# Kernel tuning notes

Hardware: AMD Instinct MI355X
Metric: run time of the kernel (lower is better)

Reference implementation:

```python
import jax, jax.numpy as jnp
import numpy as np

N, E, DIN, DOUT, NNZ = 8192, 4096, 256, 128, 65536
TEMP = float(DOUT) ** 0.5
NEG = -1e9


def setup_inputs() -> dict:
    key = jax.random.key(0)
    ks = jax.random.split(key, 8)
    stdv = 1.0 / np.sqrt(DOUT)
    u = lambda k, shp: jax.random.uniform(k, shp, jnp.float32, -stdv, stdv)
    x = jax.random.normal(ks[0], (N, DIN), jnp.float32)
    nodes = jax.random.randint(ks[1], (NNZ,), 0, N, jnp.int32)
    edges = jax.random.randint(ks[2], (NNZ,), 0, E, jnp.int32)
    hyperedge_index = jnp.stack([nodes, edges])  # [2, nnz]
    return {
        "x": x,
        "weight": u(ks[3], (DIN, DOUT)),   # transfer weight
        "weight2": u(ks[4], (DIN, DOUT)),
        "weight3": u(ks[5], (DOUT, DOUT)),
        "bias": u(ks[6], (DOUT,)),
        "q_ctx": u(ks[7], (DOUT,)),        # word_context.weight[0]
        "hyperedge_index": hyperedge_index,
        "num_nodes": N,
        "num_edges": E,
    }


def reference(x, weight, weight2, weight3, bias, q_ctx, hyperedge_index, num_nodes, num_edges):
    # dense incidence H[node, edge] = 1  (hyperedge_preprocess)
    H = jnp.zeros((num_nodes, num_edges), x.dtype).at[
        hyperedge_index[0], hyperedge_index[1]].set(1.0)
    adj = H.T                       # [E, N]  (mask / original attention for attn1)

    x4 = x @ weight2                # [N, D]  x_4att
    xt = x @ weight + bias          # [N, D]  transferred features (v of attn1)

    # ---- attention1: query = shared word-context vector, keys = x4 ----
    row = (q_ctx / TEMP) @ x4.T                    # [N] (q1 rows are identical)
    scores1 = jnp.where(adj == 0, NEG, row[None, :])  # [E, N]
    att1 = jax.nn.softmax(adj, axis=-1) + jax.nn.softmax(scores1, axis=-1)
    edge = att1 @ xt                               # [E, D]

    att2he = att1.T                                # [N, E]

    # ---- attention2: queries = x4, keys = edge @ W3 ----
    edge4 = edge @ weight3                         # [E, D]
    scores2 = jnp.where(adj.T == 0, NEG, (x4 / TEMP) @ edge4.T)  # [N, E]
    att2hn = jax.nn.softmax(adj.T, axis=-1) + jax.nn.softmax(scores2, axis=-1)

    # ---- fused outer-product attention and output projection ----
    A = att2he @ att2he.T + att2hn @ att2hn.T      # [N, N]
    h_prime_g = jax.nn.elu(A @ x4)                 # [N, D]
    return h_prime_g
```

## Files before the change

kernel.cpp:

```cpp
#include <hip/hip_runtime.h>
#include <math.h>

constexpr int Nn   = 8192;
constexpr int Ee   = 4096;
constexpr int DIN  = 256;
constexpr int DOUT = 128;
constexpr int NNZ  = 65536;
constexpr int EC   = 96;
constexpr int NC   = 48;

#define TEMPR 0.08838834764831845f
#define EM1   1.7182818284590452f


typedef __attribute__((ext_vector_type(8))) short short8;
typedef __attribute__((ext_vector_type(4))) float f32x4;

static __device__ __forceinline__ float wave_sum64(float v) {
#pragma unroll
    for (int m = 32; m; m >>= 1) v += __shfl_xor(v, m, 64);
    return v;
}
static __device__ __forceinline__ float wave_max64(float v) {
#pragma unroll
    for (int m = 32; m; m >>= 1) v = fmaxf(v, __shfl_xor(v, m, 64));
    return v;
}
static __device__ __forceinline__ short f2bf(float f) {
    union { float f; unsigned u; } v; v.f = f;
    const unsigned r = (v.u + 0x7FFFu + ((v.u >> 16) & 1u)) >> 16;
    return (short)r;
}
static __device__ __forceinline__ unsigned packbf2(float a, float b) {
    return ((unsigned)(unsigned short)f2bf(a)) |
           (((unsigned)(unsigned short)f2bf(b)) << 16);
}
static __device__ __forceinline__ float2 unpackbf2(unsigned u) {
    union { unsigned u; float f; } lo, hi;
    lo.u = u << 16; hi.u = u & 0xFFFF0000u;
    return make_float2(lo.f, hi.f);
}

__global__ __launch_bounds__(256) void k_ww3(
    const float* __restrict__ W, const float* __restrict__ W2,
    const float* __restrict__ W3, const float* __restrict__ bias,
    short* __restrict__ W2T, short* __restrict__ WWT, float* __restrict__ bW3,
    uint4* __restrict__ zb, unsigned zTot16)
{
    const int b = blockIdx.x;
    const int t = threadIdx.x;
    if (b < 32) {
        __shared__ float sW[8][128];
        const int r0 = b * 8;
        for (int i = t; i < 1024; i += 256)
            sW[i >> 7][i & 127] = W[(size_t)(r0 + (i >> 7)) * DOUT + (i & 127)];
        __syncthreads();
        const int c  = t & 127;
        const int rh = (t >> 7) * 4;
        float acc[4] = {0.f, 0.f, 0.f, 0.f};
        for (int k = 0; k < 128; ++k) {
            const float w3 = W3[(size_t)k * DOUT + c];
#pragma unroll
            for (int i = 0; i < 4; ++i) acc[i] = fmaf(sW[rh + i][k], w3, acc[i]);
        }
#pragma unroll
        for (int i = 0; i < 4; ++i)
            WWT[(size_t)c * DIN + (r0 + rh + i)] = f2bf(acc[i]);
    } else if (b < 40) {
        const int k0 = (b - 32) * 32;
        for (int i = t; i < 32 * 128; i += 256) {
            const int k = k0 + (i >> 7);
            const int n = i & 127;
            W2T[(size_t)n * DIN + k] = f2bf(W2[(size_t)k * DOUT + n]);
        }
    } else if (b == 40) {
        if (t < 128) {
            float acc = 0.f;
            for (int k = 0; k < 128; ++k)
                acc = fmaf(bias[k], W3[(size_t)k * DOUT + t], acc);
            bW3[t] = acc;
        }
    } else {
        uint4 z; z.x = z.y = z.z = z.w = 0u;
        for (unsigned i = (unsigned)(b - 41) * 256u + t; i < zTot16;
             i += 64u * 256u)
            zb[i] = z;
    }
}

__global__ __launch_bounds__(256) void k_gemm1f(
    const float* __restrict__ x, const short* __restrict__ W2T,
    const short* __restrict__ WWT, const float* __restrict__ bW3,
    const float* __restrict__ q, const int* __restrict__ hidx,
    unsigned* __restrict__ bitmap, int* __restrict__ degE, int* __restrict__ degN,
    int* __restrict__ csrEn, int* __restrict__ csrNe, int* __restrict__ csrNs,
    unsigned* __restrict__ x4b, uint2* __restrict__ xfb,
    float* __restrict__ rowv)
{
    __shared__ float srow[16];
    const int t    = threadIdx.x;
    const int lane = t & 63;
    const int wv   = t >> 6;
    const int n16  = lane & 15;
    const int quad = lane >> 4;
    const int r0   = blockIdx.x * 16;
    const int n0   = wv * 32;

    const unsigned gid = blockIdx.x * 256 + t;
    if (gid < NNZ) {
        const int n = hidx[gid];
        const int e = hidx[NNZ + gid];
        const unsigned word = (unsigned)n * (unsigned)Ee + (unsigned)e;
        const unsigned bit  = 1u << (word & 31u);
        const unsigned old  = atomicOr(&bitmap[word >> 5], bit);
        if (!(old & bit)) {
            const int pe = atomicAdd(&degE[e], 1);
            if (pe < EC) {
                csrEn[e * EC + pe] = n;
                const int pn = atomicAdd(&degN[n], 1);
                if (pn < NC) {
                    csrNe[n * NC + pn] = e;
                    csrNs[n * NC + pn] = e * EC + pe;
                }
            }
        }
    }

    f32x4 acc4[2], accw[2];
#pragma unroll
    for (int nt = 0; nt < 2; ++nt) {
        acc4[nt] = (f32x4){0.f, 0.f, 0.f, 0.f};
        accw[nt] = (f32x4){0.f, 0.f, 0.f, 0.f};
    }
#pragma unroll
    for (int k0 = 0; k0 < DIN; k0 += 32) {
        const int kb = k0 + quad * 8;
        const float4 xa = *(const float4*)&x[(size_t)(r0 + n16) * DIN + kb];
        const float4 xb = *(const float4*)&x[(size_t)(r0 + n16) * DIN + kb + 4];
        short8 af;
        af[0] = f2bf(xa.x); af[1] = f2bf(xa.y); af[2] = f2bf(xa.z); af[3] = f2bf(xa.w);
        af[4] = f2bf(xb.x); af[5] = f2bf(xb.y); af[6] = f2bf(xb.z); af[7] = f2bf(xb.w);
#pragma unroll
        for (int nt = 0; nt < 2; ++nt) {
            const int col = n0 + nt * 16 + n16;
            const short8 b4 = *(const short8*)&W2T[(size_t)col * DIN + kb];
            const short8 bw = *(const short8*)&WWT[(size_t)col * DIN + kb];
            acc4[nt] = __builtin_amdgcn_mfma_f32_16x16x32_bf16(af, b4, acc4[nt], 0, 0, 0);
            accw[nt] = __builtin_amdgcn_mfma_f32_16x16x32_bf16(af, bw, accw[nt], 0, 0, 0);
        }
    }

    float bwv[2], qv[2];
#pragma unroll
    for (int nt = 0; nt < 2; ++nt) {
        const int col = n0 + nt * 16 + n16;
        bwv[nt] = bW3[col];
        qv[nt]  = q[col];
    }
    const int s = wv * 16 + n16;
#pragma unroll
    for (int reg = 0; reg < 4; ++reg) {
        const int row = r0 + quad * 4 + reg;
        const unsigned p4 = packbf2(acc4[0][reg], acc4[1][reg]);
        const unsigned pw = packbf2(accw[0][reg] + bwv[0],
                                    accw[1][reg] + bwv[1]);
        x4b[(size_t)row * 64 + s] = p4;
        xfb[(size_t)row * 64 + s] = make_uint2(p4, pw);
    }
    float pr[4];
#pragma unroll
    for (int reg = 0; reg < 4; ++reg)
        pr[reg] = qv[0] * acc4[0][reg] + qv[1] * acc4[1][reg];
#pragma unroll
    for (int m = 8; m; m >>= 1) {
#pragma unroll
        for (int reg = 0; reg < 4; ++reg) pr[reg] += __shfl_xor(pr[reg], m, 64);
    }
    if (t < 16) srow[t] = 0.f;
    __syncthreads();
    if (n16 == 0) {
#pragma unroll
        for (int reg = 0; reg < 4; ++reg) atomicAdd(&srow[quad * 4 + reg], pr[reg]);
    }
    __syncthreads();
    if (t < 16) rowv[r0 + t] = srow[t] * TEMPR;
}

__global__ __launch_bounds__(256) void k_reduxA(
    const uint2* __restrict__ xfb, const int* __restrict__ degE,
    float* __restrict__ csx4, float* __restrict__ csxw, float* __restrict__ c2g)
{
    const int t    = threadIdx.x;
    const int lane = t & 63;
    const int w    = t >> 6;
    const int b    = blockIdx.x;
    float2 a4 = {0.f, 0.f}, aw = {0.f, 0.f};
    for (int k = 0; k < 32; ++k) {
        const int n = b * 128 + w + k * 4;
        const uint2 u = xfb[(size_t)n * 64 + lane];
        const float2 fv = unpackbf2(u.x);
        const float2 tv = unpackbf2(u.y);
        a4.x += fv.x; a4.y += fv.y;
        aw.x += tv.x; aw.y += tv.y;
    }
    atomicAdd(&csx4[lane * 2 + 0], a4.x); atomicAdd(&csx4[lane * 2 + 1], a4.y);
    atomicAdd(&csxw[lane * 2 + 0], aw.x); atomicAdd(&csxw[lane * 2 + 1], aw.y);

    const int gid = b * 256 + t;
    if (gid < Ee) {
        const int de = min(degE[gid], EC);
        const float ue = de ? 1.0f / ((float)Nn + (float)de * EM1)
                            : 2.0f / (float)Nn;
        const float v = wave_sum64(ue * ue);
        if (lane == 0) atomicAdd(c2g, v);
    }
}

__global__ __launch_bounds__(128, 6) void k_edge1(
    const int* __restrict__ degE, const int* __restrict__ csrEn,
    const float* __restrict__ rowv,
    const float* __restrict__ csx4, const float* __restrict__ csxw,
    const uint2* __restrict__ xfb,
    float* __restrict__ Sval, unsigned* __restrict__ e4b, uint2* __restrict__ GGb,
    float* __restrict__ wsArr)
{
    __shared__ int   sN[2][EC];
    __shared__ float sS[2][EC];
    const int t    = threadIdx.x;
    const int w    = t >> 6;
    const int lane = t & 63;
    const int e    = blockIdx.x * 2 + w;
    const int deg  = min(degE[e], EC);
    const float ue = deg ? 1.0f / ((float)Nn + (float)deg * EM1) : 2.0f / (float)Nn;

    int   n0 = 0, n1 = 0;
    float r0 = -INFINITY, r1 = -INFINITY;
    if (lane < deg)      { n0 = csrEn[e * EC + lane];      r0 = rowv[n0]; }
    if (lane + 64 < deg) { n1 = csrEn[e * EC + lane + 64]; r1 = rowv[n1]; }
    const float m  = wave_max64(fmaxf(r0, r1));
    const float e0 = (lane < deg)      ? expf(r0 - m) : 0.f;
    const float e1 = (lane + 64 < deg) ? expf(r1 - m) : 0.f;
    const float Z  = wave_sum64(e0 + e1);
    const float inv = deg ? 1.0f / Z : 0.f;
    const float base = EM1 * ue;
    if (lane < deg) {
        const float sv = fmaf(e0, inv, base);
        sN[w][lane] = n0; sS[w][lane] = sv;
        Sval[e * EC + lane] = sv;
        atomicAdd(&wsArr[n0], ue * sv);
    }
    if (lane + 64 < deg) {
        const float sv = fmaf(e1, inv, base);
        sN[w][lane + 64] = n1; sS[w][lane + 64] = sv;
        Sval[e * EC + lane + 64] = sv;
        atomicAdd(&wsArr[n1], ue * sv);
    }

    const float2 cw = *(const float2*)&csxw[lane * 2];
    const float2 c4 = *(const float2*)&csx4[lane * 2];
    float2 aE = make_float2(ue * cw.x, ue * cw.y);
    float2 aG = make_float2(ue * c4.x, ue * c4.y);
    int j = 0;
    for (; j + 8 <= deg; j += 8) {
        int ai[8]; float bi[8]; uint2 fu[8];
#pragma unroll
        for (int k = 0; k < 8; ++k) { ai[k] = sN[w][j+k]; bi[k] = sS[w][j+k]; }
#pragma unroll
        for (int k = 0; k < 8; ++k) fu[k] = xfb[(size_t)ai[k] * 64 + lane];
#pragma unroll
        for (int k = 0; k < 8; ++k) {
            const float2 fv = unpackbf2(fu[k].x);
            const float2 tv = unpackbf2(fu[k].y);
            aE.x = fmaf(bi[k], tv.x, aE.x); aE.y = fmaf(bi[k], tv.y, aE.y);
            aG.x = fmaf(bi[k], fv.x, aG.x); aG.y = fmaf(bi[k], fv.y, aG.y);
        }
    }
    for (; j < deg; ++j) {
        const int   a = sN[w][j];
        const float b = sS[w][j];
        const uint2 u = xfb[(size_t)a * 64 + lane];
        const float2 fv = unpackbf2(u.x);
        const float2 tv = unpackbf2(u.y);
        aE.x = fmaf(b, tv.x, aE.x); aE.y = fmaf(b, tv.y, aE.y);
        aG.x = fmaf(b, fv.x, aG.x); aG.y = fmaf(b, fv.y, aG.y);
    }
    e4b[(size_t)e * 64 + lane] = packbf2(aE.x, aE.y);
    GGb[(size_t)e * 64 + lane].x = packbf2(aG.x, aG.y);
}

__global__ __launch_bounds__(256) void k_nodeB(
    const int* __restrict__ degN, const int* __restrict__ csrNe,
    const int* __restrict__ csrNs, const unsigned* __restrict__ x4b,
    const unsigned* __restrict__ e4b, const float* __restrict__ wsArr,
    float* __restrict__ Tval,
    float* __restrict__ vxg, float* __restrict__ twg, float* __restrict__ wsg)
{
    const int t    = threadIdx.x;
    const int w    = t >> 6;
    const int lane = t & 63;
    const int b    = blockIdx.x;

    if (b < 64) {
        float2 av = {0.f, 0.f}, at2 = {0.f, 0.f}, aw = {0.f, 0.f};
        for (int k = 0; k < 32; ++k) {
            const int n   = b * 128 + w + k * 4;
            const int deg = min(degN[n], NC);
            const float vn = deg ? 1.0f / ((float)Ee + (float)deg * EM1)
                                 : 2.0f / (float)Ee;
            const float tw = deg ? fmaf((float)deg * EM1, vn, 1.0f) : 0.f;
            const float wsn = wsArr[n];
            const float2 xv = unpackbf2(x4b[(size_t)n * 64 + lane]);
            av.x  = fmaf(vn,  xv.x, av.x);  av.y  = fmaf(vn,  xv.y, av.y);
            at2.x = fmaf(tw,  xv.x, at2.x); at2.y = fmaf(tw,  xv.y, at2.y);
            aw.x  = fmaf(wsn, xv.x, aw.x);  aw.y  = fmaf(wsn, xv.y, aw.y);
        }
        atomicAdd(&vxg[lane*2+0], av.x);  atomicAdd(&vxg[lane*2+1], av.y);
        atomicAdd(&twg[lane*2+0], at2.x); atomicAdd(&twg[lane*2+1], at2.y);
        atomicAdd(&wsg[lane*2+0], aw.x);  atomicAdd(&wsg[lane*2+1], aw.y);
        return;
    }

    const int es   = lane >> 3;
    const int dl   = lane & 7;
    const int n    = (b - 64) * 4 + w;
    const int deg  = min(degN[n], NC);
    if (!deg) return;
    const float vn = 1.0f / ((float)Ee + (float)deg * EM1);

    const uint4* xr = (const uint4*)&x4b[(size_t)n * 64];
    const uint4 xua = xr[dl * 2], xub = xr[dl * 2 + 1];
    const float2 x0 = unpackbf2(xua.x), x1 = unpackbf2(xua.y),
                 x2 = unpackbf2(xua.z), x3 = unpackbf2(xua.w),
                 x4v = unpackbf2(xub.x), x5 = unpackbf2(xub.y),
                 x6 = unpackbf2(xub.z), x7 = unpackbf2(xub.w);

    float dps[6]; float exs[6]; int slots[6];
    float m = -INFINITY;
#pragma unroll
    for (int p = 0; p < 6; ++p) {
        dps[p] = -INFINITY; slots[p] = 0;
        if (p * 8 >= deg) continue;
        const int j = p * 8 + es;
        int ej = 0;
        if (j < deg) { ej = csrNe[n * NC + j]; slots[p] = csrNs[n * NC + j]; }
        const uint4* er = (const uint4*)&e4b[(size_t)ej * 64];
        const uint4 ea = er[dl * 2], eb = er[dl * 2 + 1];
        float d0 = 0.f, d1 = 0.f, d2 = 0.f, d3 = 0.f;
        { const float2 ev = unpackbf2(ea.x); d0 = fmaf(ev.x, x0.x, d0); d0 = fmaf(ev.y, x0.y, d0); }
        { const float2 ev = unpackbf2(ea.y); d1 = fmaf(ev.x, x1.x, d1); d1 = fmaf(ev.y, x1.y, d1); }
        { const float2 ev = unpackbf2(ea.z); d2 = fmaf(ev.x, x2.x, d2); d2 = fmaf(ev.y, x2.y, d2); }
        { const float2 ev = unpackbf2(ea.w); d3 = fmaf(ev.x, x3.x, d3); d3 = fmaf(ev.y, x3.y, d3); }
        { const float2 ev = unpackbf2(eb.x); d0 = fmaf(ev.x, x4v.x, d0); d0 = fmaf(ev.y, x4v.y, d0); }
        { const float2 ev = unpackbf2(eb.y); d1 = fmaf(ev.x, x5.x, d1); d1 = fmaf(ev.y, x5.y, d1); }
        { const float2 ev = unpackbf2(eb.z); d2 = fmaf(ev.x, x6.x, d2); d2 = fmaf(ev.y, x6.y, d2); }
        { const float2 ev = unpackbf2(eb.w); d3 = fmaf(ev.x, x7.x, d3); d3 = fmaf(ev.y, x7.y, d3); }
        float dot = (d0 + d1) + (d2 + d3);
        dot += __shfl_xor(dot, 1, 64);
        dot += __shfl_xor(dot, 2, 64);
        dot += __shfl_xor(dot, 4, 64);
        dot = (j < deg) ? dot * TEMPR : -INFINITY;
        dps[p] = dot;
        float mm = fmaxf(dot, __shfl_xor(dot, 8, 64));
        mm = fmaxf(mm, __shfl_xor(mm, 16, 64));
        mm = fmaxf(mm, __shfl_xor(mm, 32, 64));
        m = fmaxf(m, mm);
    }
    float Z = 0.f;
#pragma unroll
    for (int p = 0; p < 6; ++p) {
        exs[p] = 0.f;
        if (p * 8 >= deg) continue;
        const float ex = (p * 8 + es < deg) ? expf(dps[p] - m) : 0.f;
        exs[p] = ex;
        float sum = ex + __shfl_xor(ex, 8, 64);
        sum += __shfl_xor(sum, 16, 64);
        sum += __shfl_xor(sum, 32, 64);
        Z += sum;
    }
    const float invZ = 1.0f / Z;
#pragma unroll
    for (int p = 0; p < 6; ++p) {
        if (p * 8 >= deg) continue;
        if (dl == 0 && p * 8 + es < deg)
            Tval[slots[p]] = fmaf(EM1, vn, exs[p] * invZ);
    }
}

__global__ __launch_bounds__(128, 8) void k_g2(
    const int* __restrict__ degE, const int* __restrict__ csrEn,
    const float* __restrict__ Tval, const float* __restrict__ vxg,
    const unsigned* __restrict__ x4b, uint2* __restrict__ GGb)
{
    const int t    = threadIdx.x;
    const int w    = t >> 6;
    const int lane = t & 63;
    const int e    = blockIdx.x * 2 + w;
    const int deg  = min(degE[e], EC);
    float2 acc = *(const float2*)&vxg[lane * 2];
    int j = 0;
    for (; j + 8 <= deg; j += 8) {
        int ai[8]; float bi[8]; unsigned fu[8];
#pragma unroll
        for (int k = 0; k < 8; ++k) { ai[k] = csrEn[e*EC+j+k]; bi[k] = Tval[e*EC+j+k]; }
#pragma unroll
        for (int k = 0; k < 8; ++k)
            fu[k] = x4b[(size_t)ai[k] * 64 + lane];
#pragma unroll
        for (int k = 0; k < 8; ++k) {
            const float2 fv = unpackbf2(fu[k]);
            acc.x = fmaf(bi[k], fv.x, acc.x); acc.y = fmaf(bi[k], fv.y, acc.y);
        }
    }
    for (; j < deg; ++j) {
        const int   a = csrEn[e*EC+j];
        const float b = Tval[e*EC+j];
        const float2 fv = unpackbf2(x4b[(size_t)a * 64 + lane]);
        acc.x = fmaf(b, fv.x, acc.x); acc.y = fmaf(b, fv.y, acc.y);
    }
    GGb[(size_t)e * 64 + lane].y = packbf2(acc.x, acc.y);
}

__global__ __launch_bounds__(128, 6) void k_final(
    const int* __restrict__ degN, const int* __restrict__ csrNe,
    const int* __restrict__ csrNs, const float* __restrict__ Sval,
    const float* __restrict__ Tval,
    const float* __restrict__ c2g, const float* __restrict__ csx4,
    const float* __restrict__ wsg, const float* __restrict__ vxg,
    const float* __restrict__ twg,
    const uint2* __restrict__ GGb, float* __restrict__ out)
{
    const int t    = threadIdx.x;
    const int w    = t >> 6;
    const int lane = t & 63;
    const int n    = blockIdx.x * 2 + w;
    const int deg  = min(degN[n], NC);
    const float vn = deg ? 1.0f / ((float)Ee + (float)deg * EM1) : 2.0f / (float)Ee;
    const float c2 = *c2g;
    const float2 c4v = *(const float2*)&csx4[lane * 2];
    const float2 wsv = *(const float2*)&wsg[lane * 2];
    const float2 vxv = *(const float2*)&vxg[lane * 2];
    const float2 twv = *(const float2*)&twg[lane * 2];
    float2 acc;
    acc.x = fmaf(c2, c4v.x, wsv.x) + vn * fmaf((float)Ee, vxv.x, twv.x);
    acc.y = fmaf(c2, c4v.y, wsv.y) + vn * fmaf((float)Ee, vxv.y, twv.y);
    int j = 0;
    for (; j + 4 <= deg; j += 4) {
        int ei[4], si[4]; float sv[4], tv[4]; uint2 gg[4];
#pragma unroll
        for (int k = 0; k < 4; ++k) {
            ei[k] = csrNe[n*NC+j+k]; si[k] = csrNs[n*NC+j+k];
        }
#pragma unroll
        for (int k = 0; k < 4; ++k) {
            sv[k] = Sval[si[k]]; tv[k] = Tval[si[k]];
            gg[k] = GGb[(size_t)ei[k] * 64 + lane];
        }
#pragma unroll
        for (int k = 0; k < 4; ++k) {
            const float2 g1 = unpackbf2(gg[k].x);
            const float2 g2 = unpackbf2(gg[k].y);
            acc.x = fmaf(sv[k], g1.x, acc.x); acc.y = fmaf(sv[k], g1.y, acc.y);
            acc.x = fmaf(tv[k], g2.x, acc.x); acc.y = fmaf(tv[k], g2.y, acc.y);
        }
    }
    for (; j < deg; ++j) {
        const int ea = csrNe[n*NC+j];
        const int sa = csrNs[n*NC+j];
        const float sva = Sval[sa], tva = Tval[sa];
        const uint2 gg = GGb[(size_t)ea * 64 + lane];
        const float2 g1 = unpackbf2(gg.x);
        const float2 g2 = unpackbf2(gg.y);
        acc.x = fmaf(sva, g1.x, acc.x); acc.y = fmaf(sva, g1.y, acc.y);
        acc.x = fmaf(tva, g2.x, acc.x); acc.y = fmaf(tva, g2.y, acc.y);
    }
    acc.x = acc.x > 0.f ? acc.x : expm1f(acc.x);
    acc.y = acc.y > 0.f ? acc.y : expm1f(acc.y);
    const int lo = ((lane >> 4) << 5) + (lane & 15);
    out[(size_t)n * DOUT + lo]      = acc.x;
    out[(size_t)n * DOUT + lo + 16] = acc.y;
}

extern "C" void kernel_launch(void* const* d_in, const int* in_sizes, int n_in,
                              void* d_out, int out_size, void* d_ws, size_t ws_size,
                              hipStream_t stream)
{
    const float* x    = (const float*)d_in[0];
    const float* W    = (const float*)d_in[1];
    const float* W2   = (const float*)d_in[2];
    const float* W3   = (const float*)d_in[3];
    const float* bias = (const float*)d_in[4];
    const float* q    = (const float*)d_in[5];
    const int*   hidx = (const int*)d_in[6];
    float* out = (float*)d_out;

    char* wsp = (char*)d_ws;
    size_t o = 0;
    auto take = [&](size_t bytes) {
        size_t r = o; o += (bytes + 255) & ~(size_t)255; return r;
    };
    unsigned* bitmap = (unsigned*)(wsp + take((size_t)Nn * Ee / 8));
    int*   degE  = (int*)  (wsp + take((size_t)Ee * 4));
    int*   degN  = (int*)  (wsp + take((size_t)Nn * 4));
    float* wsArr = (float*)(wsp + take((size_t)Nn * 4));
    float* c2g   = (float*)(wsp + take(4));
    float* csx4  = (float*)(wsp + take(DOUT * 4));
    float* csxw  = (float*)(wsp + take(DOUT * 4));
    float* vxg   = (float*)(wsp + take(DOUT * 4));
    float* twg   = (float*)(wsp + take(DOUT * 4));
    float* wsg   = (float*)(wsp + take(DOUT * 4));
    const size_t zbytes = o;
    unsigned* x4b   = (unsigned*)(wsp + take((size_t)Nn * 64 * 4));
    uint2*    xfb   = (uint2*)   (wsp + take((size_t)Nn * 64 * 8));
    float*    rowv  = (float*)   (wsp + take((size_t)Nn * 4));
    int*      csrEn = (int*)     (wsp + take((size_t)Ee * EC * 4));
    float*    Sval  = (float*)   (wsp + take((size_t)Ee * EC * 4));
    float*    Tval  = (float*)   (wsp + take((size_t)Ee * EC * 4));
    int*      csrNe = (int*)     (wsp + take((size_t)Nn * NC * 4));
    int*      csrNs = (int*)     (wsp + take((size_t)Nn * NC * 4));
    unsigned* e4b   = (unsigned*)(wsp + take((size_t)Ee * 64 * 4));
    uint2*    GGb   = (uint2*)   (wsp + take((size_t)Ee * 64 * 8));
    short*    W2T   = (short*)   (wsp + take((size_t)DOUT * DIN * 2));
    short*    WWT   = (short*)   (wsp + take((size_t)DOUT * DIN * 2));
    float*    bW3   = (float*)   (wsp + take(DOUT * 4));
    (void)ws_size; (void)in_sizes; (void)n_in; (void)out_size;

    k_ww3   <<<105,       256, 0, stream>>>(W, W2, W3, bias, W2T, WWT, bW3,
                                            (uint4*)d_ws, (unsigned)(zbytes / 16));
    k_gemm1f<<<Nn / 16,   256, 0, stream>>>(x, W2T, WWT, bW3, q, hidx,
                                            bitmap, degE, degN, csrEn, csrNe, csrNs,
                                            x4b, xfb, rowv);
    k_reduxA<<<64,        256, 0, stream>>>(xfb, degE, csx4, csxw, c2g);
    k_edge1 <<<Ee / 2,    128, 0, stream>>>(degE, csrEn, rowv, csx4, csxw,
                                            xfb, Sval, e4b, GGb, wsArr);
    k_nodeB <<<64 + Nn/4, 256, 0, stream>>>(degN, csrNe, csrNs, x4b, e4b, wsArr,
                                            Tval, vxg, twg, wsg);
    k_g2    <<<Ee / 2,    128, 0, stream>>>(degE, csrEn, Tval, vxg, x4b, GGb);
    k_final <<<Nn / 2,    128, 0, stream>>>(degN, csrNe, csrNs, Sval, Tval,
                                            c2g, csx4, wsg, vxg, twg, GGb, out);
}
```

Baseline: 166.3 us.

## Fuse seven pipeline kernels into one cooperative persistent kernel with grid syncs

Replaces the chain of seven separate kernel launches with a single cooperative kernel of 512 blocks that runs each former stage in turn, separated by grid-wide barriers, using grid-stride loops where the old launches had more blocks. The aim is to remove per-launch overhead and the gaps between dependent stages. In exchange, each stage's parallelism is capped by the persistent grid size, and grid.sync costs are added. Occupancy is limited by launch bounds of two blocks per CU, and the larger combined shared-memory footprint may lower it further.

```diff
diff --git a/kernel.cpp b/kernel.cpp
--- a/kernel.cpp
+++ b/kernel.cpp
@@ -1,5 +1,8 @@
 #include <hip/hip_runtime.h>
+#include <hip/hip_cooperative_groups.h>
 #include <math.h>
+
+namespace cg = cooperative_groups;
 
 constexpr int Nn   = 8192;
 constexpr int Ee   = 4096;
@@ -8,6 +11,7 @@
 constexpr int NNZ  = 65536;
 constexpr int EC   = 96;
 constexpr int NC   = 48;
+constexpr int GRID = 512;
 
 #define TEMPR 0.08838834764831845f
 #define EM1   1.7182818284590452f
@@ -41,458 +45,413 @@
     return make_float2(lo.f, hi.f);
 }
 
-__global__ __launch_bounds__(256) void k_ww3(
-    const float* __restrict__ W, const float* __restrict__ W2,
-    const float* __restrict__ W3, const float* __restrict__ bias,
-    short* __restrict__ W2T, short* __restrict__ WWT, float* __restrict__ bW3,
-    uint4* __restrict__ zb, unsigned zTot16)
+struct KP {
+    const float* x; const float* W; const float* W2; const float* W3;
+    const float* bias; const float* q; const int* hidx;
+    unsigned* bitmap; int* degE; int* degN;
+    int* csrEn; int* csrNe; int* csrNs;
+    unsigned* x4b; uint2* xfb; float* rowv;
+    float* csx4; float* csxw; float* c2g;
+    float* wsArr; float* Sval; float* Tval;
+    unsigned* e4b; uint2* GGb;
+    short* W2T; short* WWT; float* bW3;
+    float* vxg; float* twg; float* wsg;
+    uint4* zb; unsigned zTot16;
+    float* out;
+};
+
+__global__ __launch_bounds__(256, 2) void k_fused(KP p)
 {
-    const int b = blockIdx.x;
-    const int t = threadIdx.x;
-    if (b < 32) {
-        __shared__ float sW[8][128];
-        const int r0 = b * 8;
-        for (int i = t; i < 1024; i += 256)
-            sW[i >> 7][i & 127] = W[(size_t)(r0 + (i >> 7)) * DOUT + (i & 127)];
-        __syncthreads();
-        const int c  = t & 127;
-        const int rh = (t >> 7) * 4;
-        float acc[4] = {0.f, 0.f, 0.f, 0.f};
-        for (int k = 0; k < 128; ++k) {
-            const float w3 = W3[(size_t)k * DOUT + c];
-#pragma unroll
-            for (int i = 0; i < 4; ++i) acc[i] = fmaf(sW[rh + i][k], w3, acc[i]);
-        }
-#pragma unroll
-        for (int i = 0; i < 4; ++i)
-            WWT[(size_t)c * DIN + (r0 + rh + i)] = f2bf(acc[i]);
-    } else if (b < 40) {
-        const int k0 = (b - 32) * 32;
-        for (int i = t; i < 32 * 128; i += 256) {
-            const int k = k0 + (i >> 7);
-            const int n = i & 127;
-            W2T[(size_t)n * DIN + k] = f2bf(W2[(size_t)k * DOUT + n]);
-        }
-    } else if (b == 40) {
-        if (t < 128) {
-            float acc = 0.f;
-            for (int k = 0; k < 128; ++k)
-                acc = fmaf(bias[k], W3[(size_t)k * DOUT + t], acc);
-            bW3[t] = acc;
-        }
-    } else {
-        uint4 z; z.x = z.y = z.z = z.w = 0u;
-        for (unsigned i = (unsigned)(b - 41) * 256u + t; i < zTot16;
-             i += 64u * 256u)
-            zb[i] = z;
-    }
-}
-
-__global__ __launch_bounds__(256) void k_gemm1f(
-    const float* __restrict__ x, const short* __restrict__ W2T,
-    const short* __restrict__ WWT, const float* __restrict__ bW3,
-    const float* __restrict__ q, const int* __restrict__ hidx,
-    unsigned* __restrict__ bitmap, int* __restrict__ degE, int* __restrict__ degN,
-    int* __restrict__ csrEn, int* __restrict__ csrNe, int* __restrict__ csrNs,
-    unsigned* __restrict__ x4b, uint2* __restrict__ xfb,
-    float* __restrict__ rowv)
-{
-    __shared__ float srow[16];
-    const int t    = threadIdx.x;
-    const int lane = t & 63;
-    const int wv   = t >> 6;
-    const int n16  = lane & 15;
-    const int quad = lane >> 4;
-    const int r0   = blockIdx.x * 16;
-    const int n0   = wv * 32;
-
-    const unsigned gid = blockIdx.x * 256 + t;
-    if (gid < NNZ) {
-        const int n = hidx[gid];
-        const int e = hidx[NNZ + gid];
-        const unsigned word = (unsigned)n * (unsigned)Ee + (unsigned)e;
-        const unsigned bit  = 1u << (word & 31u);
-        const unsigned old  = atomicOr(&bitmap[word >> 5], bit);
-        if (!(old & bit)) {
-            const int pe = atomicAdd(&degE[e], 1);
-            if (pe < EC) {
-                csrEn[e * EC + pe] = n;
-                const int pn = atomicAdd(&degN[n], 1);
-                if (pn < NC) {
-                    csrNe[n * NC + pn] = e;
-                    csrNs[n * NC + pn] = e * EC + pe;
-                }
-            }
-        }
-    }
-
-    f32x4 acc4[2], accw[2];
-#pragma unroll
-    for (int nt = 0; nt < 2; ++nt) {
-        acc4[nt] = (f32x4){0.f, 0.f, 0.f, 0.f};
-        accw[nt] = (f32x4){0.f, 0.f, 0.f, 0.f};
-    }
-#pragma unroll
-    for (int k0 = 0; k0 < DIN; k0 += 32) {
-        const int kb = k0 + quad * 8;
-        const float4 xa = *(const float4*)&x[(size_t)(r0 + n16) * DIN + kb];
-        const float4 xb = *(const float4*)&x[(size_t)(r0 + n16) * DIN + kb + 4];
-        short8 af;
-        af[0] = f2bf(xa.x); af[1] = f2bf(xa.y); af[2] = f2bf(xa.z); af[3] = f2bf(xa.w);
-        af[4] = f2bf(xb.x); af[5] = f2bf(xb.y); af[6] = f2bf(xb.z); af[7] = f2bf(xb.w);
-#pragma unroll
-        for (int nt = 0; nt < 2; ++nt) {
-            const int col = n0 + nt * 16 + n16;
-            const short8 b4 = *(const short8*)&W2T[(size_t)col * DIN + kb];
-            const short8 bw = *(const short8*)&WWT[(size_t)col * DIN + kb];
-            acc4[nt] = __builtin_amdgcn_mfma_f32_16x16x32_bf16(af, b4, acc4[nt], 0, 0, 0);
-            accw[nt] = __builtin_amdgcn_mfma_f32_16x16x32_bf16(af, bw, accw[nt], 0, 0, 0);
-        }
-    }
-
-    float bwv[2], qv[2];
-#pragma unroll
-    for (int nt = 0; nt < 2; ++nt) {
-        const int col = n0 + nt * 16 + n16;
-        bwv[nt] = bW3[col];
-        qv[nt]  = q[col];
-    }
-    const int s = wv * 16 + n16;
-#pragma unroll
-    for (int reg = 0; reg < 4; ++reg) {
-        const int row = r0 + quad * 4 + reg;
-        const unsigned p4 = packbf2(acc4[0][reg], acc4[1][reg]);
-        const unsigned pw = packbf2(accw[0][reg] + bwv[0],
-                                    accw[1][reg] + bwv[1]);
-        x4b[(size_t)row * 64 + s] = p4;
-        xfb[(size_t)row * 64 + s] = make_uint2(p4, pw);
-    }
-    float pr[4];
-#pragma unroll
-    for (int reg = 0; reg < 4; ++reg)
-        pr[reg] = qv[0] * acc4[0][reg] + qv[1] * acc4[1][reg];
-#pragma unroll
-    for (int m = 8; m; m >>= 1) {
-#pragma unroll
-        for (int reg = 0; reg < 4; ++reg) pr[reg] += __shfl_xor(pr[reg], m, 64);
-    }
-    if (t < 16) srow[t] = 0.f;
-    __syncthreads();
-    if (n16 == 0) {
-#pragma unroll
-        for (int reg = 0; reg < 4; ++reg) atomicAdd(&srow[quad * 4 + reg], pr[reg]);
-    }
-    __syncthreads();
-    if (t < 16) rowv[r0 + t] = srow[t] * TEMPR;
-}
-
-__global__ __launch_bounds__(256) void k_reduxA(
-    const uint2* __restrict__ xfb, const int* __restrict__ degE,
-    float* __restrict__ csx4, float* __restrict__ csxw, float* __restrict__ c2g)
-{
+    cg::grid_group grid = cg::this_grid();
+    const int bid  = blockIdx.x;
     const int t    = threadIdx.x;
     const int lane = t & 63;
     const int w    = t >> 6;
-    const int b    = blockIdx.x;
-    float2 a4 = {0.f, 0.f}, aw = {0.f, 0.f};
-    for (int k = 0; k < 32; ++k) {
-        const int n = b * 128 + w + k * 4;
-        const uint2 u = xfb[(size_t)n * 64 + lane];
-        const float2 fv = unpackbf2(u.x);
-        const float2 tv = unpackbf2(u.y);
-        a4.x += fv.x; a4.y += fv.y;
-        aw.x += tv.x; aw.y += tv.y;
-    }
-    atomicAdd(&csx4[lane * 2 + 0], a4.x); atomicAdd(&csx4[lane * 2 + 1], a4.y);
-    atomicAdd(&csxw[lane * 2 + 0], aw.x); atomicAdd(&csxw[lane * 2 + 1], aw.y);
-
-    const int gid = b * 256 + t;
-    if (gid < Ee) {
-        const int de = min(degE[gid], EC);
-        const float ue = de ? 1.0f / ((float)Nn + (float)de * EM1)
-                            : 2.0f / (float)Nn;
-        const float v = wave_sum64(ue * ue);
-        if (lane == 0) atomicAdd(c2g, v);
-    }
-}
-
-__global__ __launch_bounds__(128, 6) void k_edge1(
-    const int* __restrict__ degE, const int* __restrict__ csrEn,
-    const float* __restrict__ rowv,
-    const float* __restrict__ csx4, const float* __restrict__ csxw,
-    const uint2* __restrict__ xfb,
-    float* __restrict__ Sval, unsigned* __restrict__ e4b, uint2* __restrict__ GGb,
-    float* __restrict__ wsArr)
-{
-    __shared__ int   sN[2][EC];
-    __shared__ float sS[2][EC];
-    const int t    = threadIdx.x;
-    const int w    = t >> 6;
-    const int lane = t & 63;
-    const int e    = blockIdx.x * 2 + w;
-    const int deg  = min(degE[e], EC);
-    const float ue = deg ? 1.0f / ((float)Nn + (float)deg * EM1) : 2.0f / (float)Nn;
-
-    int   n0 = 0, n1 = 0;
-    float r0 = -INFINITY, r1 = -INFINITY;
-    if (lane < deg)      { n0 = csrEn[e * EC + lane];      r0 = rowv[n0]; }
-    if (lane + 64 < deg) { n1 = csrEn[e * EC + lane + 64]; r1 = rowv[n1]; }
-    const float m  = wave_max64(fmaxf(r0, r1));
-    const float e0 = (lane < deg)      ? expf(r0 - m) : 0.f;
-    const float e1 = (lane + 64 < deg) ? expf(r1 - m) : 0.f;
-    const float Z  = wave_sum64(e0 + e1);
-    const float inv = deg ? 1.0f / Z : 0.f;
-    const float base = EM1 * ue;
-    if (lane < deg) {
-        const float sv = fmaf(e0, inv, base);
-        sN[w][lane] = n0; sS[w][lane] = sv;
-        Sval[e * EC + lane] = sv;
-        atomicAdd(&wsArr[n0], ue * sv);
-    }
-    if (lane + 64 < deg) {
-        const float sv = fmaf(e1, inv, base);
-        sN[w][lane + 64] = n1; sS[w][lane + 64] = sv;
-        Sval[e * EC + lane + 64] = sv;
-        atomicAdd(&wsArr[n1], ue * sv);
-    }
-
-    const float2 cw = *(const float2*)&csxw[lane * 2];
-    const float2 c4 = *(const float2*)&csx4[lane * 2];
-    float2 aE = make_float2(ue * cw.x, ue * cw.y);
-    float2 aG = make_float2(ue * c4.x, ue * c4.y);
-    int j = 0;
-    for (; j + 8 <= deg; j += 8) {
-        int ai[8]; float bi[8]; uint2 fu[8];
-#pragma unroll
-        for (int k = 0; k < 8; ++k) { ai[k] = sN[w][j+k]; bi[k] = sS[w][j+k]; }
-#pragma unroll
-        for (int k = 0; k < 8; ++k) fu[k] = xfb[(size_t)ai[k] * 64 + lane];
-#pragma unroll
-        for (int k = 0; k < 8; ++k) {
-            const float2 fv = unpackbf2(fu[k].x);
-            const float2 tv = unpackbf2(fu[k].y);
-            aE.x = fmaf(bi[k], tv.x, aE.x); aE.y = fmaf(bi[k], tv.y, aE.y);
-            aG.x = fmaf(bi[k], fv.x, aG.x); aG.y = fmaf(bi[k], fv.y, aG.y);
-        }
-    }
-    for (; j < deg; ++j) {
-        const int   a = sN[w][j];
-        const float b = sS[w][j];
-        const uint2 u = xfb[(size_t)a * 64 + lane];
-        const float2 fv = unpackbf2(u.x);
-        const float2 tv = unpackbf2(u.y);
-        aE.x = fmaf(b, tv.x, aE.x); aE.y = fmaf(b, tv.y, aE.y);
-        aG.x = fmaf(b, fv.x, aG.x); aG.y = fmaf(b, fv.y, aG.y);
-    }
-    e4b[(size_t)e * 64 + lane] = packbf2(aE.x, aE.y);
-    GGb[(size_t)e * 64 + lane].x = packbf2(aG.x, aG.y);
-}
-
-__global__ __launch_bounds__(256) void k_nodeB(
-    const int* __restrict__ degN, const int* __restrict__ csrNe,
-    const int* __restrict__ csrNs, const unsigned* __restrict__ x4b,
-    const unsigned* __restrict__ e4b, const float* __restrict__ wsArr,
-    float* __restrict__ Tval,
-    float* __restrict__ vxg, float* __restrict__ twg, float* __restrict__ wsg)
-{
-    const int t    = threadIdx.x;
-    const int w    = t >> 6;
-    const int lane = t & 63;
-    const int b    = blockIdx.x;
-
-    if (b < 64) {
-        float2 av = {0.f, 0.f}, at2 = {0.f, 0.f}, aw = {0.f, 0.f};
+
+    __shared__ float sW[8][128];
+    __shared__ float srow[16];
+    __shared__ int   sN[4][EC];
+    __shared__ float sS[4][EC];
+
+    {
+        uint4 z; z.x = z.y = z.z = z.w = 0u;
+        for (unsigned i = (unsigned)bid * 256u + t; i < p.zTot16;
+             i += (unsigned)GRID * 256u)
+            p.zb[i] = z;
+        if (bid < 32) {
+            const int r0 = bid * 8;
+            for (int i = t; i < 1024; i += 256)
+                sW[i >> 7][i & 127] = p.W[(size_t)(r0 + (i >> 7)) * DOUT + (i & 127)];
+            __syncthreads();
+            const int c  = t & 127;
+            const int rh = (t >> 7) * 4;
+            float acc[4] = {0.f, 0.f, 0.f, 0.f};
+            for (int k = 0; k < 128; ++k) {
+                const float w3 = p.W3[(size_t)k * DOUT + c];
+#pragma unroll
+                for (int i = 0; i < 4; ++i) acc[i] = fmaf(sW[rh + i][k], w3, acc[i]);
+            }
+#pragma unroll
+            for (int i = 0; i < 4; ++i)
+                p.WWT[(size_t)c * DIN + (r0 + rh + i)] = f2bf(acc[i]);
+        } else if (bid < 40) {
+            const int k0 = (bid - 32) * 32;
+            for (int i = t; i < 32 * 128; i += 256) {
+                const int k = k0 + (i >> 7);
+                const int n = i & 127;
+                p.W2T[(size_t)n * DIN + k] = f2bf(p.W2[(size_t)k * DOUT + n]);
+            }
+        } else if (bid == 40) {
+            if (t < 128) {
+                float acc = 0.f;
+                for (int k = 0; k < 128; ++k)
+                    acc = fmaf(p.bias[k], p.W3[(size_t)k * DOUT + t], acc);
+                p.bW3[t] = acc;
+            }
+        }
+    }
+    grid.sync();
+
+    {
+        const int n16  = lane & 15;
+        const int quad = lane >> 4;
+        const int r0   = bid * 16;
+        const int n0   = w * 32;
+
+        const unsigned gid = (unsigned)bid * 256u + t;
+        if (gid < NNZ) {
+            const int n = p.hidx[gid];
+            const int e = p.hidx[NNZ + gid];
+            const unsigned word = (unsigned)n * (unsigned)Ee + (unsigned)e;
+            const unsigned bit  = 1u << (word & 31u);
+            const unsigned old  = atomicOr(&p.bitmap[word >> 5], bit);
+            if (!(old & bit)) {
+                const int pe = atomicAdd(&p.degE[e], 1);
+                if (pe < EC) {
+                    p.csrEn[e * EC + pe] = n;
+                    const int pn = atomicAdd(&p.degN[n], 1);
+                    if (pn < NC) {
+                        p.csrNe[n * NC + pn] = e;
+                        p.csrNs[n * NC + pn] = e * EC + pe;
+                    }
+                }
+            }
+        }
+
+        f32x4 acc4[2], accw[2];
+#pragma unroll
+        for (int nt = 0; nt < 2; ++nt) {
+            acc4[nt] = (f32x4){0.f, 0.f, 0.f, 0.f};
+            accw[nt] = (f32x4){0.f, 0.f, 0.f, 0.f};
+        }
+#pragma unroll
+        for (int k0 = 0; k0 < DIN; k0 += 32) {
+            const int kb = k0 + quad * 8;
+            const float4 xa = *(const float4*)&p.x[(size_t)(r0 + n16) * DIN + kb];
+            const float4 xb = *(const float4*)&p.x[(size_t)(r0 + n16) * DIN + kb + 4];
+            short8 af;
+            af[0] = f2bf(xa.x); af[1] = f2bf(xa.y); af[2] = f2bf(xa.z); af[3] = f2bf(xa.w);
+            af[4] = f2bf(xb.x); af[5] = f2bf(xb.y); af[6] = f2bf(xb.z); af[7] = f2bf(xb.w);
+#pragma unroll
+            for (int nt = 0; nt < 2; ++nt) {
+                const int col = n0 + nt * 16 + n16;
+                const short8 b4 = *(const short8*)&p.W2T[(size_t)col * DIN + kb];
+                const short8 bw = *(const short8*)&p.WWT[(size_t)col * DIN + kb];
+                acc4[nt] = __builtin_amdgcn_mfma_f32_16x16x32_bf16(af, b4, acc4[nt], 0, 0, 0);
+                accw[nt] = __builtin_amdgcn_mfma_f32_16x16x32_bf16(af, bw, accw[nt], 0, 0, 0);
+            }
+        }
+
+        float bwv[2], qv[2];
+#pragma unroll
+        for (int nt = 0; nt < 2; ++nt) {
+            const int col = n0 + nt * 16 + n16;
+            bwv[nt] = p.bW3[col];
+            qv[nt]  = p.q[col];
+        }
+        const int s = w * 16 + n16;
+#pragma unroll
+        for (int reg = 0; reg < 4; ++reg) {
+            const int row = r0 + quad * 4 + reg;
+            const unsigned p4 = packbf2(acc4[0][reg], acc4[1][reg]);
+            const unsigned pw = packbf2(accw[0][reg] + bwv[0],
+                                        accw[1][reg] + bwv[1]);
+            p.x4b[(size_t)row * 64 + s] = p4;
+            p.xfb[(size_t)row * 64 + s] = make_uint2(p4, pw);
+        }
+        float pr[4];
+#pragma unroll
+        for (int reg = 0; reg < 4; ++reg)
+            pr[reg] = qv[0] * acc4[0][reg] + qv[1] * acc4[1][reg];
+#pragma unroll
+        for (int m = 8; m; m >>= 1) {
+#pragma unroll
+            for (int reg = 0; reg < 4; ++reg) pr[reg] += __shfl_xor(pr[reg], m, 64);
+        }
+        if (t < 16) srow[t] = 0.f;
+        __syncthreads();
+        if (n16 == 0) {
+#pragma unroll
+            for (int reg = 0; reg < 4; ++reg) atomicAdd(&srow[quad * 4 + reg], pr[reg]);
+        }
+        __syncthreads();
+        if (t < 16) p.rowv[r0 + t] = srow[t] * TEMPR;
+    }
+    grid.sync();
+
+    if (bid < 64) {
+        float2 a4 = {0.f, 0.f}, aw = {0.f, 0.f};
         for (int k = 0; k < 32; ++k) {
-            const int n   = b * 128 + w + k * 4;
-            const int deg = min(degN[n], NC);
-            const float vn = deg ? 1.0f / ((float)Ee + (float)deg * EM1)
-                                 : 2.0f / (float)Ee;
-            const float tw = deg ? fmaf((float)deg * EM1, vn, 1.0f) : 0.f;
-            const float wsn = wsArr[n];
-            const float2 xv = unpackbf2(x4b[(size_t)n * 64 + lane]);
-            av.x  = fmaf(vn,  xv.x, av.x);  av.y  = fmaf(vn,  xv.y, av.y);
-            at2.x = fmaf(tw,  xv.x, at2.x); at2.y = fmaf(tw,  xv.y, at2.y);
-            aw.x  = fmaf(wsn, xv.x, aw.x);  aw.y  = fmaf(wsn, xv.y, aw.y);
-        }
-        atomicAdd(&vxg[lane*2+0], av.x);  atomicAdd(&vxg[lane*2+1], av.y);
-        atomicAdd(&twg[lane*2+0], at2.x); atomicAdd(&twg[lane*2+1], at2.y);
-        atomicAdd(&wsg[lane*2+0], aw.x);  atomicAdd(&wsg[lane*2+1], aw.y);
-        return;
-    }
-
-    const int es   = lane >> 3;
-    const int dl   = lane & 7;
-    const int n    = (b - 64) * 4 + w;
-    const int deg  = min(degN[n], NC);
-    if (!deg) return;
-    const float vn = 1.0f / ((float)Ee + (float)deg * EM1);
-
-    const uint4* xr = (const uint4*)&x4b[(size_t)n * 64];
-    const uint4 xua = xr[dl * 2], xub = xr[dl * 2 + 1];
-    const float2 x0 = unpackbf2(xua.x), x1 = unpackbf2(xua.y),
-                 x2 = unpackbf2(xua.z), x3 = unpackbf2(xua.w),
-                 x4v = unpackbf2(xub.x), x5 = unpackbf2(xub.y),
-                 x6 = unpackbf2(xub.z), x7 = unpackbf2(xub.w);
-
-    float dps[6]; float exs[6]; int slots[6];
-    float m = -INFINITY;
-#pragma unroll
-    for (int p = 0; p < 6; ++p) {
-        dps[p] = -INFINITY; slots[p] = 0;
-        if (p * 8 >= deg) continue;
-        const int j = p * 8 + es;
-        int ej = 0;
-        if (j < deg) { ej = csrNe[n * NC + j]; slots[p] = csrNs[n * NC + j]; }
-        const uint4* er = (const uint4*)&e4b[(size_t)ej * 64];
-        const uint4 ea = er[dl * 2], eb = er[dl * 2 + 1];
-        float d0 = 0.f, d1 = 0.f, d2 = 0.f, d3 = 0.f;
-        { const float2 ev = unpackbf2(ea.x); d0 = fmaf(ev.x, x0.x, d0); d0 = fmaf(ev.y, x0.y, d0); }
-        { const float2 ev = unpackbf2(ea.y); d1 = fmaf(ev.x, x1.x, d1); d1 = fmaf(ev.y, x1.y, d1); }
-        { const float2 ev = unpackbf2(ea.z); d2 = fmaf(ev.x, x2.x, d2); d2 = fmaf(ev.y, x2.y, d2); }
-        { const float2 ev = unpackbf2(ea.w); d3 = fmaf(ev.x, x3.x, d3); d3 = fmaf(ev.y, x3.y, d3); }
-        { const float2 ev = unpackbf2(eb.x); d0 = fmaf(ev.x, x4v.x, d0); d0 = fmaf(ev.y, x4v.y, d0); }
-        { const float2 ev = unpackbf2(eb.y); d1 = fmaf(ev.x, x5.x, d1); d1 = fmaf(ev.y, x5.y, d1); }
-        { const float2 ev = unpackbf2(eb.z); d2 = fmaf(ev.x, x6.x, d2); d2 = fmaf(ev.y, x6.y, d2); }
-        { const float2 ev = unpackbf2(eb.w); d3 = fmaf(ev.x, x7.x, d3); d3 = fmaf(ev.y, x7.y, d3); }
-        float dot = (d0 + d1) + (d2 + d3);
-        dot += __shfl_xor(dot, 1, 64);
-        dot += __shfl_xor(dot, 2, 64);
-        dot += __shfl_xor(dot, 4, 64);
-        dot = (j < deg) ? dot * TEMPR : -INFINITY;
-        dps[p] = dot;
-        float mm = fmaxf(dot, __shfl_xor(dot, 8, 64));
-        mm = fmaxf(mm, __shfl_xor(mm, 16, 64));
-        mm = fmaxf(mm, __shfl_xor(mm, 32, 64));
-        m = fmaxf(m, mm);
-    }
-    float Z = 0.f;
-#pragma unroll
-    for (int p = 0; p < 6; ++p) {
-        exs[p] = 0.f;
-        if (p * 8 >= deg) continue;
-        const float ex = (p * 8 + es < deg) ? expf(dps[p] - m) : 0.f;
-        exs[p] = ex;
-        float sum = ex + __shfl_xor(ex, 8, 64);
-        sum += __shfl_xor(sum, 16, 64);
-        sum += __shfl_xor(sum, 32, 64);
-        Z += sum;
-    }
-    const float invZ = 1.0f / Z;
-#pragma unroll
-    for (int p = 0; p < 6; ++p) {
-        if (p * 8 >= deg) continue;
-        if (dl == 0 && p * 8 + es < deg)
-            Tval[slots[p]] = fmaf(EM1, vn, exs[p] * invZ);
-    }
-}
-
-__global__ __launch_bounds__(128, 8) void k_g2(
-    const int* __restrict__ degE, const int* __restrict__ csrEn,
-    const float* __restrict__ Tval, const float* __restrict__ vxg,
-    const unsigned* __restrict__ x4b, uint2* __restrict__ GGb)
-{
-    const int t    = threadIdx.x;
-    const int w    = t >> 6;
-    const int lane = t & 63;
-    const int e    = blockIdx.x * 2 + w;
-    const int deg  = min(degE[e], EC);
-    float2 acc = *(const float2*)&vxg[lane * 2];
-    int j = 0;
-    for (; j + 8 <= deg; j += 8) {
-        int ai[8]; float bi[8]; unsigned fu[8];
-#pragma unroll
-        for (int k = 0; k < 8; ++k) { ai[k] = csrEn[e*EC+j+k]; bi[k] = Tval[e*EC+j+k]; }
-#pragma unroll
-        for (int k = 0; k < 8; ++k)
-            fu[k] = x4b[(size_t)ai[k] * 64 + lane];
-#pragma unroll
-        for (int k = 0; k < 8; ++k) {
-            const float2 fv = unpackbf2(fu[k]);
-            acc.x = fmaf(bi[k], fv.x, acc.x); acc.y = fmaf(bi[k], fv.y, acc.y);
-        }
-    }
-    for (; j < deg; ++j) {
-        const int   a = csrEn[e*EC+j];
-        const float b = Tval[e*EC+j];
-        const float2 fv = unpackbf2(x4b[(size_t)a * 64 + lane]);
-        acc.x = fmaf(b, fv.x, acc.x); acc.y = fmaf(b, fv.y, acc.y);
-    }
-    GGb[(size_t)e * 64 + lane].y = packbf2(acc.x, acc.y);
-}
-
-__global__ __launch_bounds__(128, 6) void k_final(
-    const int* __restrict__ degN, const int* __restrict__ csrNe,
-    const int* __restrict__ csrNs, const float* __restrict__ Sval,
-    const float* __restrict__ Tval,
-    const float* __restrict__ c2g, const float* __restrict__ csx4,
-    const float* __restrict__ wsg, const float* __restrict__ vxg,
-    const float* __restrict__ twg,
-    const uint2* __restrict__ GGb, float* __restrict__ out)
-{
-    const int t    = threadIdx.x;
-    const int w    = t >> 6;
-    const int lane = t & 63;
-    const int n    = blockIdx.x * 2 + w;
-    const int deg  = min(degN[n], NC);
-    const float vn = deg ? 1.0f / ((float)Ee + (float)deg * EM1) : 2.0f / (float)Ee;
-    const float c2 = *c2g;
-    const float2 c4v = *(const float2*)&csx4[lane * 2];
-    const float2 wsv = *(const float2*)&wsg[lane * 2];
-    const float2 vxv = *(const float2*)&vxg[lane * 2];
-    const float2 twv = *(const float2*)&twg[lane * 2];
-    float2 acc;
-    acc.x = fmaf(c2, c4v.x, wsv.x) + vn * fmaf((float)Ee, vxv.x, twv.x);
-    acc.y = fmaf(c2, c4v.y, wsv.y) + vn * fmaf((float)Ee, vxv.y, twv.y);
-    int j = 0;
-    for (; j + 4 <= deg; j += 4) {
-        int ei[4], si[4]; float sv[4], tv[4]; uint2 gg[4];
-#pragma unroll
-        for (int k = 0; k < 4; ++k) {
-            ei[k] = csrNe[n*NC+j+k]; si[k] = csrNs[n*NC+j+k];
-        }
-#pragma unroll
-        for (int k = 0; k < 4; ++k) {
-            sv[k] = Sval[si[k]]; tv[k] = Tval[si[k]];
-            gg[k] = GGb[(size_t)ei[k] * 64 + lane];
-        }
-#pragma unroll
-        for (int k = 0; k < 4; ++k) {
-            const float2 g1 = unpackbf2(gg[k].x);
-            const float2 g2 = unpackbf2(gg[k].y);
-            acc.x = fmaf(sv[k], g1.x, acc.x); acc.y = fmaf(sv[k], g1.y, acc.y);
-            acc.x = fmaf(tv[k], g2.x, acc.x); acc.y = fmaf(tv[k], g2.y, acc.y);
-        }
-    }
-    for (; j < deg; ++j) {
-        const int ea = csrNe[n*NC+j];
-        const int sa = csrNs[n*NC+j];
-        const float sva = Sval[sa], tva = Tval[sa];
-        const uint2 gg = GGb[(size_t)ea * 64 + lane];
-        const float2 g1 = unpackbf2(gg.x);
-        const float2 g2 = unpackbf2(gg.y);
-        acc.x = fmaf(sva, g1.x, acc.x); acc.y = fmaf(sva, g1.y, acc.y);
-        acc.x = fmaf(tva, g2.x, acc.x); acc.y = fmaf(tva, g2.y, acc.y);
-    }
-    acc.x = acc.x > 0.f ? acc.x : expm1f(acc.x);
-    acc.y = acc.y > 0.f ? acc.y : expm1f(acc.y);
-    const int lo = ((lane >> 4) << 5) + (lane & 15);
-    out[(size_t)n * DOUT + lo]      = acc.x;
-    out[(size_t)n * DOUT + lo + 16] = acc.y;
+            const int n = bid * 128 + w + k * 4;
+            const uint2 u2 = p.xfb[(size_t)n * 64 + lane];
+            const float2 fv = unpackbf2(u2.x);
+            const float2 tv = unpackbf2(u2.y);
+            a4.x += fv.x; a4.y += fv.y;
+            aw.x += tv.x; aw.y += tv.y;
+        }
+        atomicAdd(&p.csx4[lane * 2 + 0], a4.x); atomicAdd(&p.csx4[lane * 2 + 1], a4.y);
+        atomicAdd(&p.csxw[lane * 2 + 0], aw.x); atomicAdd(&p.csxw[lane * 2 + 1], aw.y);
+
+        const int gid = bid * 256 + t;
+        if (gid < Ee) {
+            const int de = min(p.degE[gid], EC);
+            const float ue = de ? 1.0f / ((float)Nn + (float)de * EM1)
+                                : 2.0f / (float)Nn;
+            const float v = wave_sum64(ue * ue);
+            if (lane == 0) atomicAdd(p.c2g, v);
+        }
+    }
+    grid.sync();
+
+    for (int u = bid; u < Ee / 4; u += GRID) {
+        const int e   = u * 4 + w;
+        const int deg = min(p.degE[e], EC);
+        const float ue = deg ? 1.0f / ((float)Nn + (float)deg * EM1) : 2.0f / (float)Nn;
+
+        int   n0 = 0, n1 = 0;
+        float r0 = -INFINITY, r1 = -INFINITY;
+        if (lane < deg)      { n0 = p.csrEn[e * EC + lane];      r0 = p.rowv[n0]; }
+        if (lane + 64 < deg) { n1 = p.csrEn[e * EC + lane + 64]; r1 = p.rowv[n1]; }
+        const float m  = wave_max64(fmaxf(r0, r1));
+        const float e0 = (lane < deg)      ? expf(r0 - m) : 0.f;
+        const float e1 = (lane + 64 < deg) ? expf(r1 - m) : 0.f;
+        const float Z  = wave_sum64(e0 + e1);
+        const float inv = deg ? 1.0f / Z : 0.f;
+        const float base = EM1 * ue;
+        if (lane < deg) {
+            const float sv = fmaf(e0, inv, base);
+            sN[w][lane] = n0; sS[w][lane] = sv;
+            p.Sval[e * EC + lane] = sv;
+            atomicAdd(&p.wsArr[n0], ue * sv);
+        }
+        if (lane + 64 < deg) {
+            const float sv = fmaf(e1, inv, base);
+            sN[w][lane + 64] = n1; sS[w][lane + 64] = sv;
+            p.Sval[e * EC + lane + 64] = sv;
+            atomicAdd(&p.wsArr[n1], ue * sv);
+        }
+
+        const float2 cw = *(const float2*)&p.csxw[lane * 2];
+        const float2 c4 = *(const float2*)&p.csx4[lane * 2];
+        float2 aE = make_float2(ue * cw.x, ue * cw.y);
+        float2 aG = make_float2(ue * c4.x, ue * c4.y);
+        int j = 0;
+        for (; j + 8 <= deg; j += 8) {
+            int ai[8]; float bi[8]; uint2 fu[8];
+#pragma unroll
+            for (int k = 0; k < 8; ++k) { ai[k] = sN[w][j+k]; bi[k] = sS[w][j+k]; }
+#pragma unroll
+            for (int k = 0; k < 8; ++k) fu[k] = p.xfb[(size_t)ai[k] * 64 + lane];
+#pragma unroll
+            for (int k = 0; k < 8; ++k) {
+                const float2 fv = unpackbf2(fu[k].x);
+                const float2 tv = unpackbf2(fu[k].y);
+                aE.x = fmaf(bi[k], tv.x, aE.x); aE.y = fmaf(bi[k], tv.y, aE.y);
+                aG.x = fmaf(bi[k], fv.x, aG.x); aG.y = fmaf(bi[k], fv.y, aG.y);
+            }
+        }
+        for (; j < deg; ++j) {
+            const int   a = sN[w][j];
+            const float b = sS[w][j];
+            const uint2 u2 = p.xfb[(size_t)a * 64 + lane];
+            const float2 fv = unpackbf2(u2.x);
+            const float2 tv = unpackbf2(u2.y);
+            aE.x = fmaf(b, tv.x, aE.x); aE.y = fmaf(b, tv.y, aE.y);
+            aG.x = fmaf(b, fv.x, aG.x); aG.y = fmaf(b, fv.y, aG.y);
+        }
+        p.e4b[(size_t)e * 64 + lane] = packbf2(aE.x, aE.y);
+        p.GGb[(size_t)e * 64 + lane].x = packbf2(aG.x, aG.y);
+    }
+    grid.sync();
+
+    for (int u = bid; u < 64 + Nn / 4; u += GRID) {
+        if (u < 64) {
+            float2 av = {0.f, 0.f}, at2 = {0.f, 0.f}, aw = {0.f, 0.f};
+            for (int k = 0; k < 32; ++k) {
+                const int n   = u * 128 + w + k * 4;
+                const int deg = min(p.degN[n], NC);
+                const float vn = deg ? 1.0f / ((float)Ee + (float)deg * EM1)
+                                     : 2.0f / (float)Ee;
+                const float tw = deg ? fmaf((float)deg * EM1, vn, 1.0f) : 0.f;
+                const float wsn = p.wsArr[n];
+                const float2 xv = unpackbf2(p.x4b[(size_t)n * 64 + lane]);
+                av.x  = fmaf(vn,  xv.x, av.x);  av.y  = fmaf(vn,  xv.y, av.y);
+                at2.x = fmaf(tw,  xv.x, at2.x); at2.y = fmaf(tw,  xv.y, at2.y);
+                aw.x  = fmaf(wsn, xv.x, aw.x);  aw.y  = fmaf(wsn, xv.y, aw.y);
+            }
+            atomicAdd(&p.vxg[lane*2+0], av.x);  atomicAdd(&p.vxg[lane*2+1], av.y);
+            atomicAdd(&p.twg[lane*2+0], at2.x); atomicAdd(&p.twg[lane*2+1], at2.y);
+            atomicAdd(&p.wsg[lane*2+0], aw.x);  atomicAdd(&p.wsg[lane*2+1], aw.y);
+        } else {
+            const int es   = lane >> 3;
+            const int dl   = lane & 7;
+            const int n    = (u - 64) * 4 + w;
+            const int deg  = min(p.degN[n], NC);
+            if (deg) {
+                const float vn = 1.0f / ((float)Ee + (float)deg * EM1);
+                const uint4* xr = (const uint4*)&p.x4b[(size_t)n * 64];
+                const uint4 xua = xr[dl * 2], xub = xr[dl * 2 + 1];
+                const float2 x0 = unpackbf2(xua.x), x1 = unpackbf2(xua.y),
+                             x2 = unpackbf2(xua.z), x3 = unpackbf2(xua.w),
+                             x4v = unpackbf2(xub.x), x5 = unpackbf2(xub.y),
+                             x6 = unpackbf2(xub.z), x7 = unpackbf2(xub.w);
+                float dps[6]; float exs[6]; int slots[6];
+                float m = -INFINITY;
+#pragma unroll
+                for (int q6 = 0; q6 < 6; ++q6) {
+                    dps[q6] = -INFINITY; slots[q6] = 0;
+                    if (q6 * 8 >= deg) continue;
+                    const int j = q6 * 8 + es;
+                    int ej = 0;
+                    if (j < deg) { ej = p.csrNe[n * NC + j]; slots[q6] = p.csrNs[n * NC + j]; }
+                    const uint4* er = (const uint4*)&p.e4b[(size_t)ej * 64];
+                    const uint4 ea = er[dl * 2], eb = er[dl * 2 + 1];
+                    float d0 = 0.f, d1 = 0.f, d2 = 0.f, d3 = 0.f;
+                    { const float2 ev = unpackbf2(ea.x); d0 = fmaf(ev.x, x0.x, d0); d0 = fmaf(ev.y, x0.y, d0); }
+                    { const float2 ev = unpackbf2(ea.y); d1 = fmaf(ev.x, x1.x, d1); d1 = fmaf(ev.y, x1.y, d1); }
+                    { const float2 ev = unpackbf2(ea.z); d2 = fmaf(ev.x, x2.x, d2); d2 = fmaf(ev.y, x2.y, d2); }
+                    { const float2 ev = unpackbf2(ea.w); d3 = fmaf(ev.x, x3.x, d3); d3 = fmaf(ev.y, x3.y, d3); }
+                    { const float2 ev = unpackbf2(eb.x); d0 = fmaf(ev.x, x4v.x, d0); d0 = fmaf(ev.y, x4v.y, d0); }
+                    { const float2 ev = unpackbf2(eb.y); d1 = fmaf(ev.x, x5.x, d1); d1 = fmaf(ev.y, x5.y, d1); }
+                    { const float2 ev = unpackbf2(eb.z); d2 = fmaf(ev.x, x6.x, d2); d2 = fmaf(ev.y, x6.y, d2); }
+                    { const float2 ev = unpackbf2(eb.w); d3 = fmaf(ev.x, x7.x, d3); d3 = fmaf(ev.y, x7.y, d3); }
+                    float dot = (d0 + d1) + (d2 + d3);
+                    dot += __shfl_xor(dot, 1, 64);
+                    dot += __shfl_xor(dot, 2, 64);
+                    dot += __shfl_xor(dot, 4, 64);
+                    dot = (j < deg) ? dot * TEMPR : -INFINITY;
+                    dps[q6] = dot;
+                    float mm = fmaxf(dot, __shfl_xor(dot, 8, 64));
+                    mm = fmaxf(mm, __shfl_xor(mm, 16, 64));
+                    mm = fmaxf(mm, __shfl_xor(mm, 32, 64));
+                    m = fmaxf(m, mm);
+                }
+                float Z = 0.f;
+#pragma unroll
+                for (int q6 = 0; q6 < 6; ++q6) {
+                    exs[q6] = 0.f;
+                    if (q6 * 8 >= deg) continue;
+                    const float ex = (q6 * 8 + es < deg) ? expf(dps[q6] - m) : 0.f;
+                    exs[q6] = ex;
+                    float sum = ex + __shfl_xor(ex, 8, 64);
+                    sum += __shfl_xor(sum, 16, 64);
+                    sum += __shfl_xor(sum, 32, 64);
+                    Z += sum;
+                }
+                const float invZ = 1.0f / Z;
+#pragma unroll
+                for (int q6 = 0; q6 < 6; ++q6) {
+                    if (q6 * 8 >= deg) continue;
+                    if (dl == 0 && q6 * 8 + es < deg)
+                        p.Tval[slots[q6]] = fmaf(EM1, vn, exs[q6] * invZ);
+                }
+            }
+        }
+    }
+    grid.sync();
+
+    for (int u = bid; u < Ee / 4; u += GRID) {
+        const int e   = u * 4 + w;
+        const int deg = min(p.degE[e], EC);
+        float2 acc = *(const float2*)&p.vxg[lane * 2];
+        int j = 0;
+        for (; j + 8 <= deg; j += 8) {
+            int ai[8]; float bi[8]; unsigned fu[8];
+#pragma unroll
+            for (int k = 0; k < 8; ++k) { ai[k] = p.csrEn[e*EC+j+k]; bi[k] = p.Tval[e*EC+j+k]; }
+#pragma unroll
+            for (int k = 0; k < 8; ++k)
+                fu[k] = p.x4b[(size_t)ai[k] * 64 + lane];
+#pragma unroll
+            for (int k = 0; k < 8; ++k) {
+                const float2 fv = unpackbf2(fu[k]);
+                acc.x = fmaf(bi[k], fv.x, acc.x); acc.y = fmaf(bi[k], fv.y, acc.y);
+            }
+        }
+        for (; j < deg; ++j) {
+            const int   a = p.csrEn[e*EC+j];
+            const float b = p.Tval[e*EC+j];
+            const float2 fv = unpackbf2(p.x4b[(size_t)a * 64 + lane]);
+            acc.x = fmaf(b, fv.x, acc.x); acc.y = fmaf(b, fv.y, acc.y);
+        }
+        p.GGb[(size_t)e * 64 + lane].y = packbf2(acc.x, acc.y);
+    }
+    grid.sync();
+
+    for (int u = bid; u < Nn / 4; u += GRID) {
+        const int n   = u * 4 + w;
+        const int deg = min(p.degN[n], NC);
+        const float vn = deg ? 1.0f / ((float)Ee + (float)deg * EM1) : 2.0f / (float)Ee;
+        const float c2 = *p.c2g;
+        const float2 c4v = *(const float2*)&p.csx4[lane * 2];
+        const float2 wsv = *(const float2*)&p.wsg[lane * 2];
+        const float2 vxv = *(const float2*)&p.vxg[lane * 2];
+        const float2 twv = *(const float2*)&p.twg[lane * 2];
+        float2 acc;
+        acc.x = fmaf(c2, c4v.x, wsv.x) + vn * fmaf((float)Ee, vxv.x, twv.x);
+        acc.y = fmaf(c2, c4v.y, wsv.y) + vn * fmaf((float)Ee, vxv.y, twv.y);
+        int j = 0;
+        for (; j + 4 <= deg; j += 4) {
+            int ei[4], si[4]; float sv[4], tv[4]; uint2 gg[4];
+#pragma unroll
+            for (int k = 0; k < 4; ++k) {
+                ei[k] = p.csrNe[n*NC+j+k]; si[k] = p.csrNs[n*NC+j+k];
+            }
+#pragma unroll
+            for (int k = 0; k < 4; ++k) {
+                sv[k] = p.Sval[si[k]]; tv[k] = p.Tval[si[k]];
+                gg[k] = p.GGb[(size_t)ei[k] * 64 + lane];
+            }
+#pragma unroll
+            for (int k = 0; k < 4; ++k) {
+                const float2 g1 = unpackbf2(gg[k].x);
+                const float2 g2 = unpackbf2(gg[k].y);
+                acc.x = fmaf(sv[k], g1.x, acc.x); acc.y = fmaf(sv[k], g1.y, acc.y);
+                acc.x = fmaf(tv[k], g2.x, acc.x); acc.y = fmaf(tv[k], g2.y, acc.y);
+            }
+        }
+        for (; j < deg; ++j) {
+            const int ea = p.csrNe[n*NC+j];
+            const int sa = p.csrNs[n*NC+j];
+            const float sva = p.Sval[sa], tva = p.Tval[sa];
+            const uint2 gg = p.GGb[(size_t)ea * 64 + lane];
+            const float2 g1 = unpackbf2(gg.x);
+            const float2 g2 = unpackbf2(gg.y);
+            acc.x = fmaf(sva, g1.x, acc.x); acc.y = fmaf(sva, g1.y, acc.y);
+            acc.x = fmaf(tva, g2.x, acc.x); acc.y = fmaf(tva, g2.y, acc.y);
+        }
+        acc.x = acc.x > 0.f ? acc.x : expm1f(acc.x);
+        acc.y = acc.y > 0.f ? acc.y : expm1f(acc.y);
+        const int lo = ((lane >> 4) << 5) + (lane & 15);
+        p.out[(size_t)n * DOUT + lo]      = acc.x;
+        p.out[(size_t)n * DOUT + lo + 16] = acc.y;
+    }
 }
 
 extern "C" void kernel_launch(void* const* d_in, const int* in_sizes, int n_in,
                               void* d_out, int out_size, void* d_ws, size_t ws_size,
                               hipStream_t stream)
 {
-    const float* x    = (const float*)d_in[0];
-    const float* W    = (const float*)d_in[1];
-    const float* W2   = (const float*)d_in[2];
-    const float* W3   = (const float*)d_in[3];
-    const float* bias = (const float*)d_in[4];
-    const float* q    = (const float*)d_in[5];
-    const int*   hidx = (const int*)d_in[6];
-    float* out = (float*)d_out;
-
     char* wsp = (char*)d_ws;
     size_t o = 0;
     auto take = [&](size_t bytes) {
@@ -524,17 +483,26 @@
     float*    bW3   = (float*)   (wsp + take(DOUT * 4));
     (void)ws_size; (void)in_sizes; (void)n_in; (void)out_size;
 
-    k_ww3   <<<105,       256, 0, stream>>>(W, W2, W3, bias, W2T, WWT, bW3,
-                                            (uint4*)d_ws, (unsigned)(zbytes / 16));
-    k_gemm1f<<<Nn / 16,   256, 0, stream>>>(x, W2T, WWT, bW3, q, hidx,
-                                            bitmap, degE, degN, csrEn, csrNe, csrNs,
-                                            x4b, xfb, rowv);
-    k_reduxA<<<64,        256, 0, stream>>>(xfb, degE, csx4, csxw, c2g);
-    k_edge1 <<<Ee / 2,    128, 0, stream>>>(degE, csrEn, rowv, csx4, csxw,
-                                            xfb, Sval, e4b, GGb, wsArr);
-    k_nodeB <<<64 + Nn/4, 256, 0, stream>>>(degN, csrNe, csrNs, x4b, e4b, wsArr,
-                                            Tval, vxg, twg, wsg);
-    k_g2    <<<Ee / 2,    128, 0, stream>>>(degE, csrEn, Tval, vxg, x4b, GGb);
-    k_final <<<Nn / 2,    128, 0, stream>>>(degN, csrNe, csrNs, Sval, Tval,
-                                            c2g, csx4, wsg, vxg, twg, GGb, out);
-}
+    KP p;
+    p.x = (const float*)d_in[0];
+    p.W = (const float*)d_in[1];
+    p.W2 = (const float*)d_in[2];
+    p.W3 = (const float*)d_in[3];
+    p.bias = (const float*)d_in[4];
+    p.q = (const float*)d_in[5];
+    p.hidx = (const int*)d_in[6];
+    p.bitmap = bitmap; p.degE = degE; p.degN = degN;
+    p.csrEn = csrEn; p.csrNe = csrNe; p.csrNs = csrNs;
+    p.x4b = x4b; p.xfb = xfb; p.rowv = rowv;
+    p.csx4 = csx4; p.csxw = csxw; p.c2g = c2g;
+    p.wsArr = wsArr; p.Sval = Sval; p.Tval = Tval;
+    p.e4b = e4b; p.GGb = GGb;
+    p.W2T = W2T; p.WWT = WWT; p.bW3 = bW3;
+    p.vxg = vxg; p.twg = twg; p.wsg = wsg;
+    p.zb = (uint4*)d_ws; p.zTot16 = (unsigned)(zbytes / 16);
+    p.out = (float*)d_out;
+
+    void* kargs[] = { (void*)&p };
+    hipLaunchCooperativeKernel((const void*)k_fused, dim3(GRID), dim3(256),
+                               kargs, 0, stream);
+}
```

After: 522.4 us. 214% more time.
